# Kernel tuning notes

Measured on AMD Instinct MI355X. Metric: run time of the kernel, lower is better.

Reference implementation:

```python
import jax, jax.numpy as jnp
import numpy as np

B, S, D, H = 4, 2048, 768, 12
DH = D // H
SPARSITY = 0.5


def make_random_mask(key, seq_len, sparsity=SPARSITY):
    # Faithful to create_random_mask: uniform matrix, diagonal forced to 1,
    # top-k per row kept, diagonal forced on again.
    rand = jax.random.uniform(key, (seq_len, seq_len), dtype=jnp.float32)
    eye = jnp.eye(seq_len, dtype=bool)
    rand = jnp.where(eye, 1.0, rand)
    k = int(seq_len * (1.0 - sparsity))
    _, idx = jax.lax.top_k(rand, k)  # [S, k]
    mask = jnp.zeros((seq_len, seq_len), dtype=bool)
    rows = jnp.arange(seq_len)[:, None]
    mask = mask.at[rows, idx].set(True)
    mask = mask | eye
    return mask


def setup_inputs() -> dict:
    key = jax.random.key(0)
    ks = jax.random.split(key, 6)
    scale = 1.0 / np.sqrt(D)
    inp = {
        "hidden_states": jax.random.normal(ks[0], (B, S, D), dtype=jnp.float32),
        "Wq": jax.random.normal(ks[1], (D, D), dtype=jnp.float32) * scale,
        "bq": jnp.zeros((D,), dtype=jnp.float32),
        "Wk": jax.random.normal(ks[2], (D, D), dtype=jnp.float32) * scale,
        "bk": jnp.zeros((D,), dtype=jnp.float32),
        "Wv": jax.random.normal(ks[3], (D, D), dtype=jnp.float32) * scale,
        "bv": jnp.zeros((D,), dtype=jnp.float32),
        "Wo": jax.random.normal(ks[4], (D, D), dtype=jnp.float32) * scale,
        "bo": jnp.zeros((D,), dtype=jnp.float32),
        "random_mask": make_random_mask(ks[5], S),
    }
    return inp


def reference(hidden_states, Wq, bq, Wk, bk, Wv, bv, Wo, bo, random_mask):
    b, s, d = hidden_states.shape
    q = (hidden_states @ Wq + bq).reshape(b, s, H, DH).transpose(0, 2, 1, 3)  # [B,H,S,dH]
    k = (hidden_states @ Wk + bk).reshape(b, s, H, DH).transpose(0, 2, 1, 3)
    v = (hidden_states @ Wv + bv).reshape(b, s, H, DH).transpose(0, 2, 1, 3)

    scores = jnp.einsum('bhqd,bhkd->bhqk', q, k) / np.sqrt(DH)  # [B,H,S,S]
    scores = jnp.where(random_mask[None, None, :, :], scores, -1e9)
    probs = jax.nn.softmax(scores, axis=-1)
    ctx = jnp.einsum('bhqk,bhkd->bhqd', probs, v)  # [B,H,S,dH]
    ctx = ctx.transpose(0, 2, 1, 3).reshape(b, s, d)
    out = ctx @ Wo + bo
    return out
```

## Files before the change

### kernel.cpp

```cpp
#include <hip/hip_runtime.h>
#include <stdint.h>


#define B_ 4
#define S_ 2048
#define D_ 768
#define H_ 12
#define DH_ 64
#define NROW (B_ * S_)
#define MW (S_ / 64)

typedef __attribute__((ext_vector_type(4))) float f32x4;
typedef __attribute__((ext_vector_type(16))) float f32x16;
typedef __attribute__((ext_vector_type(8))) __bf16 bf16x8;
typedef __attribute__((ext_vector_type(8))) unsigned short us8;
typedef __attribute__((ext_vector_type(4))) unsigned short us4;
typedef __attribute__((ext_vector_type(2))) unsigned int u32x2;

#define LOG2E 1.4426950408889634f
#define SCQ (0.125f * LOG2E)

static __device__ __forceinline__ unsigned short f2bf(float f) {
  unsigned int u = __float_as_uint(f);
  unsigned int r = (u + 0x7fffu + ((u >> 16) & 1u)) >> 16;
  return (unsigned short)r;
}

static __device__ __forceinline__ unsigned int pk2c(float lo, float hi) {
  union { unsigned int u; __bf16 h[2]; } x;
  x.h[0] = (__bf16)lo; x.h[1] = (__bf16)hi;
  return x.u;
}

static __device__ __forceinline__ u32x2 swap32(unsigned int a, unsigned int b) {
  return __builtin_amdgcn_permlane32_swap(a, b, false, false);
}
static __device__ __forceinline__ float xhalf_sum(float x) {
  u32x2 r = swap32(__float_as_uint(x), __float_as_uint(x));
  return __uint_as_float(r[0]) + __uint_as_float(r[1]);
}

static __device__ __forceinline__ void gld_lds16(const void* g, void* l) {
  __builtin_amdgcn_global_load_lds(
      (const __attribute__((address_space(1))) void*)g,
      (__attribute__((address_space(3))) void*)l, 16, 0, 0);
}

__global__ void k_cast_x(const float* __restrict__ x, unsigned short* __restrict__ xb) {
  int i = blockIdx.x * blockDim.x + threadIdx.x;
  const float4* p = (const float4*)(x + (size_t)i * 8);
  float4 a = p[0], b = p[1];
  us8 o;
  o[0] = f2bf(a.x); o[1] = f2bf(a.y); o[2] = f2bf(a.z); o[3] = f2bf(a.w);
  o[4] = f2bf(b.x); o[5] = f2bf(b.y); o[6] = f2bf(b.z); o[7] = f2bf(b.w);
  *(us8*)(xb + (size_t)i * 8) = o;
}

__global__ void k_cast_tw(const float* __restrict__ w0, const float* __restrict__ w1,
                          const float* __restrict__ w2, const float* __restrict__ w3,
                          unsigned short* __restrict__ wt) {
  __shared__ float tl[64][65];
  int z = blockIdx.z;
  const float* w = (z == 0) ? w0 : (z == 1) ? w1 : (z == 2) ? w2 : w3;
  int k0 = blockIdx.x * 64, n0 = blockIdx.y * 64;
  int t = threadIdx.x;
#pragma unroll
  for (int rr = 0; rr < 16; rr++) {
    int lin = rr * 256 + t;
    int kk = lin >> 6, nn = lin & 63;
    tl[kk][nn] = w[(size_t)(k0 + kk) * D_ + n0 + nn];
  }
  __syncthreads();
  unsigned short* o = wt + (size_t)z * D_ * D_;
#pragma unroll
  for (int rr = 0; rr < 16; rr++) {
    int lin = rr * 256 + t;
    int nn = lin >> 6, kk = lin & 63;
    o[(size_t)(n0 + nn) * D_ + k0 + kk] = f2bf(tl[kk][nn]);
  }
}

__global__ void k_maskbits(const void* __restrict__ m,
                           unsigned long long* __restrict__ mb) {
  __shared__ int sdet[4];
  int t = threadIdx.x, blk = blockIdx.x;
  unsigned int wv = ((const unsigned int*)m)[blk * 64 + (t & 63)];
  unsigned long long det = __ballot(wv > 1u);
  if ((t & 63) == 0) sdet[t >> 6] = (det != 0ull);
  __syncthreads();
  int isbyte = sdet[0] | sdet[1] | sdet[2] | sdet[3];
  int i = blk * 256 + t;
  int v = isbyte ? (int)((const unsigned char*)m)[i]
                 : (int)(((const unsigned int*)m)[i] != 0u);
  unsigned long long w = __ballot(v != 0);
  if ((t & 63) == 0) mb[i >> 6] = w;
}

template <int MODE, typename OT>
static __device__ __forceinline__ void gemm_body(const unsigned short* __restrict__ A,
                                                 const unsigned short* __restrict__ Bt,
                                                 const float* __restrict__ bias,
                                                 OT* __restrict__ out) {
  __shared__ unsigned short As[128 * 32];
  __shared__ unsigned short Bs[128 * 32];
  int t = threadIdx.x;
  int lane = t & 63, wv = t >> 6;
  int wr = wv >> 1, wc = wv & 1;
  int c = lane & 15, g = lane >> 4;
  int rowBase = blockIdx.x * 128;
  int colBase = blockIdx.y * 128;

  f32x4 acc[4][4];
#pragma unroll
  for (int i = 0; i < 4; i++)
#pragma unroll
    for (int j = 0; j < 4; j++) acc[i][j] = {0.f, 0.f, 0.f, 0.f};

  for (int k0 = 0; k0 < D_; k0 += 32) {
    __syncthreads();
#pragma unroll
    for (int i = 0; i < 2; i++) {
      int p = t + i * 256;
      int row = p >> 2, u = p & 3;
      int ch = u ^ ((row >> 1) & 3);
      gld_lds16(A + (size_t)(rowBase + row) * D_ + k0 + ch * 8, &As[p * 8]);
      gld_lds16(Bt + (size_t)(colBase + row) * D_ + k0 + ch * 8, &Bs[p * 8]);
    }
    __syncthreads();
    bf16x8 af[4], bfr[4];
#pragma unroll
    for (int f = 0; f < 4; f++) {
      int row = wr * 64 + f * 16 + c;
      int ch = g ^ ((row >> 1) & 3);
      af[f] = *(const bf16x8*)&As[row * 32 + ch * 8];
      int col = wc * 64 + f * 16 + c;
      int ch2 = g ^ ((col >> 1) & 3);
      bfr[f] = *(const bf16x8*)&Bs[col * 32 + ch2 * 8];
    }
#pragma unroll
    for (int fi = 0; fi < 4; fi++)
#pragma unroll
      for (int fj = 0; fj < 4; fj++)
        acc[fi][fj] = __builtin_amdgcn_mfma_f32_16x16x32_bf16(af[fi], bfr[fj], acc[fi][fj], 0, 0, 0);
  }
  if constexpr (MODE == 2) {
#pragma unroll
    for (int fj = 0; fj < 4; fj++) {
      int col = colBase + wc * 64 + fj * 16 + c;
      float bv_ = bias[col];
      int hh = col >> 6, dh = col & 63;
#pragma unroll
      for (int fi = 0; fi < 4; fi++) {
        int row0 = rowBase + wr * 64 + fi * 16 + g * 4;
        int bb = row0 >> 11, sq = row0 & 2047;
        us4 pk;
#pragma unroll
        for (int r = 0; r < 4; r++) pk[r] = f2bf(acc[fi][fj][r] + bv_);
        *(us4*)&((unsigned short*)out)[(size_t)((bb * H_ + hh) * DH_ + dh) * S_ + sq] = pk;
      }
    }
  } else {
#pragma unroll
    for (int fj = 0; fj < 4; fj++) {
      int col = colBase + wc * 64 + fj * 16 + c;
      float bv_ = bias[col];
#pragma unroll
      for (int fi = 0; fi < 4; fi++) {
#pragma unroll
        for (int r = 0; r < 4; r++) {
          int row = rowBase + wr * 64 + fi * 16 + g * 4 + r;
          float v = acc[fi][fj][r] + bv_;
          if constexpr (MODE == 1) v *= SCQ;
          if constexpr (sizeof(OT) == 4) {
            ((float*)out)[(size_t)row * D_ + col] = v;
          } else {
            ((unsigned short*)out)[(size_t)row * D_ + col] = f2bf(v);
          }
        }
      }
    }
  }
}

__global__ void k_gemm_qkv(const unsigned short* __restrict__ X,
                           const unsigned short* __restrict__ Wt,
                           const float* __restrict__ bq, const float* __restrict__ bk,
                           const float* __restrict__ bv,
                           unsigned short* __restrict__ Q, unsigned short* __restrict__ K,
                           unsigned short* __restrict__ Vt_out) {
  int z = blockIdx.z;
  const unsigned short* Bt = Wt + (size_t)z * D_ * D_;
  if (z == 0)       gemm_body<1, unsigned short>(X, Bt, bq, Q);
  else if (z == 1)  gemm_body<0, unsigned short>(X, Bt, bk, K);
  else              gemm_body<2, unsigned short>(X, Bt, bv, Vt_out);
}

__global__ void k_gemm_out(const unsigned short* __restrict__ C,
                           const unsigned short* __restrict__ Wto,
                           const float* __restrict__ bo, float* __restrict__ out) {
  gemm_body<0, float>(C, Wto, bo, out);
}

__launch_bounds__(256, 4)
__global__ void k_attn(const unsigned short* __restrict__ Qn,
                       const unsigned short* __restrict__ Kn,
                       const unsigned short* __restrict__ Vt,
                       const unsigned long long* __restrict__ mb,
                       unsigned short* __restrict__ ctx) {
  __shared__ unsigned short Ks[2][64 * 64];
  __shared__ unsigned short Vs[2][64 * 64];

  int t = threadIdx.x;
  int lane = t & 63, w = t >> 6;
  int half = lane >> 5, lq = lane & 31;

  int wid = (blockIdx.x & 7) * 96 + (blockIdx.x >> 3);
  int qt = wid & 15, hb = wid >> 4;
  int h = hb % H_, b = hb / H_;
  int qbase = qt * 128, qw = w * 32;
  int mq = qbase + qw + lq;
  size_t qrow = (size_t)b * S_ + mq;

  const unsigned short* Kg = Kn + (size_t)b * S_ * D_ + h * DH_;
  const unsigned short* Vg = Vt + (size_t)((b * H_ + h) * DH_) * S_;

  bf16x8 qf[4];
#pragma unroll
  for (int ksl = 0; ksl < 4; ksl++)
    qf[ksl] = *(const bf16x8*)&Qn[qrow * D_ + h * DH_ + ksl * 16 + half * 8];

  f32x16 oacc[2];
#pragma unroll
  for (int j = 0; j < 16; j++) { oacc[0][j] = 0.f; oacc[1][j] = 0.f; }
  float l = 0.f;

  auto STAGE = [&](int nb, int kt2) {
    int kb2 = kt2 * 64;
#pragma unroll
    for (int i = 0; i < 2; i++) {
      int p = t + i * 256;
      int row = p >> 3, u = p & 7;
      int ch = u ^ (row & 7);
      gld_lds16(Kg + (size_t)(kb2 + row) * D_ + ch * 8, &Ks[nb][p * 8]);
      gld_lds16(Vg + (size_t)row * S_ + kb2 + ch * 8, &Vs[nb][p * 8]);
    }
  };

  STAGE(0, 0);
  unsigned long long mw = mb[(size_t)mq * MW];
  __syncthreads();

  int buf = 0;
  for (int kt = 0; kt < S_ / 64; kt++) {
    if (kt < S_ / 64 - 1) STAGE(buf ^ 1, kt + 1);
    unsigned long long mwu = mw;
    if (kt < S_ / 64 - 1) mw = mb[(size_t)mq * MW + kt + 1];

    f32x16 sacc[2];
#pragma unroll
    for (int j = 0; j < 16; j++) { sacc[0][j] = 0.f; sacc[1][j] = 0.f; }
    __builtin_amdgcn_s_setprio(1);
#pragma unroll
    for (int sb = 0; sb < 2; sb++) {
      int kr = sb * 32 + lq;
      int sw = kr & 7;
#pragma unroll
      for (int ksl = 0; ksl < 4; ksl++) {
        int ch = (ksl * 2 + half) ^ sw;
        bf16x8 kf = *(const bf16x8*)&Ks[buf][kr * 64 + ch * 8];
        sacc[sb] = __builtin_amdgcn_mfma_f32_32x32x16_bf16(kf, qf[ksl], sacc[sb], 0, 0, 0);
      }
    }
    __builtin_amdgcn_s_setprio(0);

    unsigned int msh0 = ((unsigned int)mwu) >> (4 * half);
    unsigned int msh1 = ((unsigned int)(mwu >> 32)) >> (4 * half);
    float psa[4] = {0.f, 0.f, 0.f, 0.f};
#pragma unroll
    for (int sb = 0; sb < 2; sb++) {
#pragma unroll
      for (int r = 0; r < 16; r++) {
        int cpos = (r & 3) + 8 * (r >> 2);
        unsigned int word = (sb == 0) ? msh0 : msh1;
        float e = __builtin_amdgcn_exp2f(sacc[sb][r]);
        e = ((word >> cpos) & 1u) ? e : 0.f;
        sacc[sb][r] = e;
        psa[r & 3] += e;
      }
    }
    l += (psa[0] + psa[1]) + (psa[2] + psa[3]);

    union PaU { unsigned int w[4]; bf16x8 v; } pa[4];
#pragma unroll
    for (int sb = 0; sb < 2; sb++)
#pragma unroll
      for (int par = 0; par < 2; par++) {
        int rb = par * 8;
        unsigned int x0 = pk2c(sacc[sb][rb + 0], sacc[sb][rb + 1]);
        unsigned int x1 = pk2c(sacc[sb][rb + 2], sacc[sb][rb + 3]);
        unsigned int y0 = pk2c(sacc[sb][rb + 4], sacc[sb][rb + 5]);
        unsigned int y1 = pk2c(sacc[sb][rb + 6], sacc[sb][rb + 7]);
        u32x2 r0 = swap32(x0, y0);
        u32x2 r1 = swap32(x1, y1);
        pa[sb * 2 + par].w[0] = r0[0];
        pa[sb * 2 + par].w[1] = r1[0];
        pa[sb * 2 + par].w[2] = r0[1];
        pa[sb * 2 + par].w[3] = r1[1];
      }

    __builtin_amdgcn_s_setprio(1);
#pragma unroll
    for (int dhg = 0; dhg < 2; dhg++) {
      int dr = dhg * 32 + lq;
      int sw = lq & 7;
#pragma unroll
      for (int ks = 0; ks < 4; ks++) {
        int ch = (ks * 2 + half) ^ sw;
        bf16x8 vf = *(const bf16x8*)&Vs[buf][dr * 64 + ch * 8];
        oacc[dhg] = __builtin_amdgcn_mfma_f32_32x32x16_bf16(vf, pa[ks].v, oacc[dhg], 0, 0, 0);
      }
    }
    __builtin_amdgcn_s_setprio(0);

    __syncthreads();
    buf ^= 1;
  }

  float linv = 1.0f / xhalf_sum(l);
  size_t obase = qrow * D_ + h * DH_;
#pragma unroll
  for (int dhg = 0; dhg < 2; dhg++)
#pragma unroll
    for (int i = 0; i < 4; i++) {
      us4 pk;
#pragma unroll
      for (int r = 0; r < 4; r++) pk[r] = f2bf(oacc[dhg][i * 4 + r] * linv);
      *(us4*)&ctx[obase + dhg * 32 + i * 8 + half * 4] = pk;
    }
}

extern "C" void kernel_launch(void* const* d_in, const int* in_sizes, int n_in,
                              void* d_out, int out_size, void* d_ws, size_t ws_size,
                              hipStream_t stream) {
  const float* hs = (const float*)d_in[0];
  const float* Wq = (const float*)d_in[1];
  const float* bq = (const float*)d_in[2];
  const float* Wk = (const float*)d_in[3];
  const float* bk = (const float*)d_in[4];
  const float* Wv = (const float*)d_in[5];
  const float* bv = (const float*)d_in[6];
  const float* Wo = (const float*)d_in[7];
  const float* bo = (const float*)d_in[8];
  const void* mask = d_in[9];
  float* out = (float*)d_out;

  char* ws = (char*)d_ws;
  size_t off = 0;
  auto alloc = [&](size_t bytes) -> void* {
    void* p = ws + off;
    off += (bytes + 255) & ~(size_t)255;
    return p;
  };
  unsigned short* Xb = (unsigned short*)alloc((size_t)NROW * D_ * 2);
  unsigned short* Wt = (unsigned short*)alloc((size_t)4 * D_ * D_ * 2);
  unsigned short* Qn = (unsigned short*)alloc((size_t)NROW * D_ * 2);
  unsigned short* Kn = (unsigned short*)alloc((size_t)NROW * D_ * 2);
  unsigned short* Vtr = (unsigned short*)alloc((size_t)B_ * H_ * DH_ * S_ * 2);
  unsigned short* Cx = (unsigned short*)alloc((size_t)NROW * D_ * 2);
  unsigned long long* Mb = (unsigned long long*)alloc((size_t)S_ * MW * 8);

  k_cast_x<<<NROW * D_ / 8 / 256, 256, 0, stream>>>(hs, Xb);
  k_cast_tw<<<dim3(12, 12, 4), 256, 0, stream>>>(Wq, Wk, Wv, Wo, Wt);
  k_maskbits<<<S_ * S_ / 256, 256, 0, stream>>>(mask, Mb);
  k_gemm_qkv<<<dim3(64, 6, 3), 256, 0, stream>>>(Xb, Wt, bq, bk, bv, Qn, Kn, Vtr);
  k_attn<<<768, 256, 0, stream>>>(Qn, Kn, Vtr, Mb, Cx);
  k_gemm_out<<<dim3(64, 6, 1), 256, 0, stream>>>(Cx, Wt + (size_t)3 * D_ * D_, bo, out);
}
```

Before: 269.6 us.

## Merge prep kernels into one launch and drop setprio in attention loop

Folds the three preprocessing kernels (input cast, weight transpose-cast, mask bit-packing) into a single launch that dispatches on block index. This removes two launch gaps. The mask path now has each block handle 2048 elements, eight per thread, which cuts the block count. The attention kernel also drops its s_setprio raises around the MFMA sections, which changes wave scheduling priority and could help or hurt overlap. Byte-vs-int detection is now decided per 2048-element chunk instead of per 256 elements.

```diff
diff --git a/kernel.cpp b/kernel.cpp
--- a/kernel.cpp
+++ b/kernel.cpp
@@ -46,54 +46,76 @@
       (__attribute__((address_space(3))) void*)l, 16, 0, 0);
 }
 
-__global__ void k_cast_x(const float* __restrict__ x, unsigned short* __restrict__ xb) {
-  int i = blockIdx.x * blockDim.x + threadIdx.x;
-  const float4* p = (const float4*)(x + (size_t)i * 8);
-  float4 a = p[0], b = p[1];
-  us8 o;
-  o[0] = f2bf(a.x); o[1] = f2bf(a.y); o[2] = f2bf(a.z); o[3] = f2bf(a.w);
-  o[4] = f2bf(b.x); o[5] = f2bf(b.y); o[6] = f2bf(b.z); o[7] = f2bf(b.w);
-  *(us8*)(xb + (size_t)i * 8) = o;
-}
-
-__global__ void k_cast_tw(const float* __restrict__ w0, const float* __restrict__ w1,
-                          const float* __restrict__ w2, const float* __restrict__ w3,
-                          unsigned short* __restrict__ wt) {
+#define PREP_CASTX 3072
+#define PREP_TW 576
+#define PREP_MB 2048
+__global__ void k_prep(const float* __restrict__ hs,
+                       const float* __restrict__ w0, const float* __restrict__ w1,
+                       const float* __restrict__ w2, const float* __restrict__ w3,
+                       const void* __restrict__ mask,
+                       unsigned short* __restrict__ xb, unsigned short* __restrict__ wt,
+                       unsigned long long* __restrict__ mb) {
   __shared__ float tl[64][65];
-  int z = blockIdx.z;
-  const float* w = (z == 0) ? w0 : (z == 1) ? w1 : (z == 2) ? w2 : w3;
-  int k0 = blockIdx.x * 64, n0 = blockIdx.y * 64;
-  int t = threadIdx.x;
-#pragma unroll
-  for (int rr = 0; rr < 16; rr++) {
-    int lin = rr * 256 + t;
-    int kk = lin >> 6, nn = lin & 63;
-    tl[kk][nn] = w[(size_t)(k0 + kk) * D_ + n0 + nn];
+  int bid = blockIdx.x, t = threadIdx.x;
+
+  if (bid < PREP_CASTX) {
+    size_t i = (size_t)bid * 256 + t;
+    const float4* p = (const float4*)(hs + i * 8);
+    float4 a = p[0], b = p[1];
+    us8 o;
+    o[0] = f2bf(a.x); o[1] = f2bf(a.y); o[2] = f2bf(a.z); o[3] = f2bf(a.w);
+    o[4] = f2bf(b.x); o[5] = f2bf(b.y); o[6] = f2bf(b.z); o[7] = f2bf(b.w);
+    *(us8*)(xb + i * 8) = o;
+  } else if (bid < PREP_CASTX + PREP_TW) {
+    int tw = bid - PREP_CASTX;
+    int z = tw / 144, r2 = tw % 144;
+    int bx = r2 % 12, by = r2 / 12;
+    const float* w = (z == 0) ? w0 : (z == 1) ? w1 : (z == 2) ? w2 : w3;
+    int k0 = bx * 64, n0 = by * 64;
+#pragma unroll
+    for (int rr = 0; rr < 16; rr++) {
+      int lin = rr * 256 + t;
+      int kk = lin >> 6, nn = lin & 63;
+      tl[kk][nn] = w[(size_t)(k0 + kk) * D_ + n0 + nn];
+    }
+    __syncthreads();
+    unsigned short* o = wt + (size_t)z * D_ * D_;
+#pragma unroll
+    for (int rr = 0; rr < 16; rr++) {
+      int lin = rr * 256 + t;
+      int nn = lin >> 6, kk = lin & 63;
+      o[(size_t)(n0 + nn) * D_ + k0 + kk] = f2bf(tl[kk][nn]);
+    }
+  } else {
+    int mbid = bid - (PREP_CASTX + PREP_TW);
+    int w = t >> 6, lane = t & 63;
+    int base = mbid * 2048 + w * 512;
+    int* sdet = (int*)tl;
+    unsigned int wv[8];
+#pragma unroll
+    for (int j = 0; j < 8; j++) wv[j] = ((const unsigned int*)mask)[base + j * 64 + lane];
+    int any = 0;
+#pragma unroll
+    for (int j = 0; j < 8; j++) any |= (wv[j] > 1u) ? 1 : 0;
+    unsigned long long det = __ballot(any);
+    if (lane == 0) sdet[w] = (det != 0ull);
+    __syncthreads();
+    int isbyte = sdet[0] | sdet[1] | sdet[2] | sdet[3];
+    if (!isbyte) {
+#pragma unroll
+      for (int j = 0; j < 8; j++) {
+        unsigned long long bw = __ballot(wv[j] != 0u);
+        if (lane == 0) mb[mbid * 32 + w * 8 + j] = bw;
+      }
+    } else {
+#pragma unroll
+      for (int j = 0; j < 8; j++) {
+        unsigned char bv = ((const unsigned char*)mask)[base + j * 64 + lane];
+        unsigned long long bw = __ballot(bv != 0);
+        if (lane == 0) mb[mbid * 32 + w * 8 + j] = bw;
+      }
+    }
   }
-  __syncthreads();
-  unsigned short* o = wt + (size_t)z * D_ * D_;
-#pragma unroll
-  for (int rr = 0; rr < 16; rr++) {
-    int lin = rr * 256 + t;
-    int nn = lin >> 6, kk = lin & 63;
-    o[(size_t)(n0 + nn) * D_ + k0 + kk] = f2bf(tl[kk][nn]);
-  }
-}
-
-__global__ void k_maskbits(const void* __restrict__ m,
-                           unsigned long long* __restrict__ mb) {
-  __shared__ int sdet[4];
-  int t = threadIdx.x, blk = blockIdx.x;
-  unsigned int wv = ((const unsigned int*)m)[blk * 64 + (t & 63)];
-  unsigned long long det = __ballot(wv > 1u);
-  if ((t & 63) == 0) sdet[t >> 6] = (det != 0ull);
-  __syncthreads();
-  int isbyte = sdet[0] | sdet[1] | sdet[2] | sdet[3];
-  int i = blk * 256 + t;
-  int v = isbyte ? (int)((const unsigned char*)m)[i]
-                 : (int)(((const unsigned int*)m)[i] != 0u);
-  unsigned long long w = __ballot(v != 0);
-  if ((t & 63) == 0) mb[i >> 6] = w;
 }
 
 template <int MODE, typename OT>
@@ -259,7 +281,6 @@
     f32x16 sacc[2];
 #pragma unroll
     for (int j = 0; j < 16; j++) { sacc[0][j] = 0.f; sacc[1][j] = 0.f; }
-    __builtin_amdgcn_s_setprio(1);
 #pragma unroll
     for (int sb = 0; sb < 2; sb++) {
       int kr = sb * 32 + lq;
@@ -271,7 +292,6 @@
         sacc[sb] = __builtin_amdgcn_mfma_f32_32x32x16_bf16(kf, qf[ksl], sacc[sb], 0, 0, 0);
       }
     }
-    __builtin_amdgcn_s_setprio(0);
 
     unsigned int msh0 = ((unsigned int)mwu) >> (4 * half);
     unsigned int msh1 = ((unsigned int)(mwu >> 32)) >> (4 * half);
@@ -308,7 +328,6 @@
         pa[sb * 2 + par].w[3] = r1[1];
       }
 
-    __builtin_amdgcn_s_setprio(1);
 #pragma unroll
     for (int dhg = 0; dhg < 2; dhg++) {
       int dr = dhg * 32 + lq;
@@ -320,7 +339,6 @@
         oacc[dhg] = __builtin_amdgcn_mfma_f32_32x32x16_bf16(vf, pa[ks].v, oacc[dhg], 0, 0, 0);
       }
     }
-    __builtin_amdgcn_s_setprio(0);
 
     __syncthreads();
     buf ^= 1;
@@ -369,9 +387,7 @@
   unsigned short* Cx = (unsigned short*)alloc((size_t)NROW * D_ * 2);
   unsigned long long* Mb = (unsigned long long*)alloc((size_t)S_ * MW * 8);
 
-  k_cast_x<<<NROW * D_ / 8 / 256, 256, 0, stream>>>(hs, Xb);
-  k_cast_tw<<<dim3(12, 12, 4), 256, 0, stream>>>(Wq, Wk, Wv, Wo, Wt);
-  k_maskbits<<<S_ * S_ / 256, 256, 0, stream>>>(mask, Mb);
+  k_prep<<<PREP_CASTX + PREP_TW + PREP_MB, 256, 0, stream>>>(hs, Wq, Wk, Wv, Wo, mask, Xb, Wt, Mb);
   k_gemm_qkv<<<dim3(64, 6, 3), 256, 0, stream>>>(Xb, Wt, bq, bk, bv, Qn, Kn, Vtr);
   k_attn<<<768, 256, 0, stream>>>(Qn, Kn, Vtr, Mb, Cx);
   k_gemm_out<<<dim3(64, 6, 1), 256, 0, stream>>>(Cx, Wt + (size_t)3 * D_ * D_, bo, out);
```

Result: faster. 256.3 us (-4.9%).
